# Performance work log

Hardware: AMD Instinct MI355X
Metric: run time of the kernel (lower is better)

The kernel has to match this reference:

```python
import jax, jax.numpy as jnp
import numpy as np

CH = 64
GROUPS = 8
EPS = 1e-5


def setup_inputs() -> dict:
    key = jax.random.key(0)
    ks = jax.random.split(key, 5)
    x = jax.random.normal(ks[0], (16, CH, 256, 256), dtype=jnp.float32)
    gn_weight = jnp.ones((CH,), jnp.float32)
    gn_bias = jnp.zeros((CH,), jnp.float32)
    # 1x1 convs == per-pixel channel GEMMs; store as [C_out, C_in]
    s = 1.0 / np.sqrt(CH)
    w1 = jax.random.uniform(ks[1], (CH, CH), jnp.float32, -s, s)
    b1 = jax.random.uniform(ks[2], (CH,), jnp.float32, -s, s)
    w2 = jax.random.uniform(ks[3], (CH, CH), jnp.float32, -s, s)
    b2 = jax.random.uniform(ks[4], (CH,), jnp.float32, -s, s)
    return {"x": x, "gn_weight": gn_weight, "gn_bias": gn_bias,
            "w1": w1, "b1": b1, "w2": w2, "b2": b2}


def group_norm(x, weight, bias):
    B, C, H, W = x.shape
    g = x.reshape(B, GROUPS, C // GROUPS, H, W)
    mean = g.mean(axis=(2, 3, 4), keepdims=True)
    var = g.var(axis=(2, 3, 4), keepdims=True)
    g = (g - mean) * jax.lax.rsqrt(var + EPS)
    x = g.reshape(B, C, H, W)
    return x * weight[None, :, None, None] + bias[None, :, None, None]


def reference(x, gn_weight, gn_bias, w1, b1, w2, b2):
    # FFT2 -> IFFT2 round-trip, keep real part (identity up to float noise)
    x_ifft = jnp.fft.ifft2(jnp.fft.fft2(x, axes=(-2, -1)), axes=(-2, -1)).real
    x_norm = group_norm(x_ifft, gn_weight, gn_bias)
    # ffn: 1x1 conv -> relu -> 1x1 conv, as channel einsums
    h = jnp.einsum('oc,bchw->bohw', w1, x_norm) + b1[None, :, None, None]
    h = jax.nn.relu(h)
    h = jnp.einsum('oc,bchw->bohw', w2, h) + b2[None, :, None, None]
    return x_norm + h
```

## Files before the change

kernel.cpp:

```cpp
#include <hip/hip_runtime.h>

#define CH 64
#define HW 65536
#define NBATCH 16
#define GROUP_ELEMS (8 * HW)
#define GN_EPS 1e-5f

typedef __attribute__((ext_vector_type(8))) short bf16x8;
typedef __attribute__((ext_vector_type(4))) float f32x4;

#define WS_SUMS   0
#define WS_FRAGS  1024
#define WS_SCALE  16384
#define WS_SHIFT  17408

static __device__ __forceinline__ unsigned short f2bf(float f) {
    unsigned u = __float_as_uint(f);
    return (unsigned short)((u + 0x7fffu + ((u >> 16) & 1u)) >> 16);
}
static __device__ __forceinline__ float bf2f(unsigned h) {
    return __uint_as_float(h << 16);
}
#define SWZ(a) ((a) ^ ((((a) >> 7) & 7) << 4))

__global__ __launch_bounds__(256, 8) void gn_stats(const float* __restrict__ x,
                                                   float* __restrict__ ws) {
    const int blk = blockIdx.x, grp = blk >> 4, split = blk & 15, tid = threadIdx.x;
    const float4* x4 = (const float4*)x + (size_t)grp * (GROUP_ELEMS / 4)
                                        + (size_t)split * (GROUP_ELEMS / 64);
    float s = 0.f, ss = 0.f;
    #pragma unroll
    for (int i = 0; i < 32; ++i) {
        float4 v = x4[i * 256 + tid];
        s  += v.x + v.y + v.z + v.w;
        ss += v.x * v.x + v.y * v.y + v.z * v.z + v.w * v.w;
    }
    #pragma unroll
    for (int o = 32; o > 0; o >>= 1) {
        s += __shfl_down(s, o, 64);
        ss += __shfl_down(ss, o, 64);
    }
    if ((tid & 63) == 0) {
        atomicAdd(&ws[grp * 2 + 0], s);
        atomicAdd(&ws[grp * 2 + 1], ss);
    }
}

__global__ __launch_bounds__(64) void gn_setup(const float* __restrict__ w1,
                                               const float* __restrict__ w2,
                                               const float* __restrict__ gamma,
                                               const float* __restrict__ beta,
                                               float* __restrict__ ws) {
    const int bid = blockIdx.x, l = threadIdx.x;
    if (bid < 16) {
        const int mat = bid >> 3, mt = (bid >> 1) & 3, kt = bid & 1;
        const float* w = mat ? w2 : w1;
        const int row = mt * 16 + (l & 15);
        const float* p = w + row * 64 + kt * 32 + (l >> 4) * 8;
        unsigned hi[4], lo[4];
        #pragma unroll
        for (int j = 0; j < 4; ++j) {
            float v0 = p[2 * j], v1 = p[2 * j + 1];
            unsigned h0 = f2bf(v0), h1 = f2bf(v1);
            unsigned l0 = f2bf(v0 - bf2f(h0)), l1 = f2bf(v1 - bf2f(h1));
            hi[j] = h0 | (h1 << 16);
            lo[j] = l0 | (l1 << 16);
        }
        unsigned* fr = (unsigned*)ws + WS_FRAGS;
        const int fhi = (mat * 2 + 0) * 8 + mt * 2 + kt;
        const int flo = (mat * 2 + 1) * 8 + mt * 2 + kt;
        *(uint4*)(fr + fhi * 256 + l * 4) = make_uint4(hi[0], hi[1], hi[2], hi[3]);
        *(uint4*)(fr + flo * 256 + l * 4) = make_uint4(lo[0], lo[1], lo[2], lo[3]);
    } else {
        const int c = l, g = c >> 3;
        const float ga = gamma[c], be = beta[c], invn = 1.f / (float)GROUP_ELEMS;
        for (int b = 0; b < NBATCH; ++b) {
            float s  = ws[(b * 8 + g) * 2 + 0];
            float ss = ws[(b * 8 + g) * 2 + 1];
            float m  = s * invn;
            float var = ss * invn - m * m;
            float rs = rsqrtf(var + GN_EPS);
            float A = rs * ga;
            ws[WS_SCALE + b * 64 + c] = A;
            ws[WS_SHIFT + b * 64 + c] = be - m * A;
        }
    }
}

__global__ __launch_bounds__(256, 2) void fused_gn_ffn(
        const float* __restrict__ x,
        const float* __restrict__ b1g, const float* __restrict__ b2g,
        const float* __restrict__ ws, float* __restrict__ out) {

    __shared__ __align__(16) char lds[65536];
    const int tid = threadIdx.x, wid = tid >> 6, l = tid & 63;
    const int b = blockIdx.x >> 9;
    const int pw = (blockIdx.x & 511) * 128 + wid * 32;

    char* X_hi = lds + wid * 16384;
    char* X_lo = X_hi + 4096;
    char* H_hi = X_hi + 8192;
    char* H_lo = X_hi + 12288;

    const unsigned* fr = (const unsigned*)ws + WS_FRAGS;
    bf16x8 w1h[4][2], w1l[4][2], w2h[4][2], w2l[4][2];
    #pragma unroll
    for (int mt = 0; mt < 4; ++mt)
        #pragma unroll
        for (int kt = 0; kt < 2; ++kt) {
            w1h[mt][kt] = __builtin_bit_cast(bf16x8, *(const uint4*)(fr + (0  + mt * 2 + kt) * 256 + l * 4));
            w1l[mt][kt] = __builtin_bit_cast(bf16x8, *(const uint4*)(fr + (8  + mt * 2 + kt) * 256 + l * 4));
            w2h[mt][kt] = __builtin_bit_cast(bf16x8, *(const uint4*)(fr + (16 + mt * 2 + kt) * 256 + l * 4));
            w2l[mt][kt] = __builtin_bit_cast(bf16x8, *(const uint4*)(fr + (24 + mt * 2 + kt) * 256 + l * 4));
        }

    f32x4 b1v[4], b2v[4];
    #pragma unroll
    for (int mt = 0; mt < 4; ++mt) {
        const int r = mt * 16 + (l >> 4) * 4;
        b1v[mt] = *(const f32x4*)(b1g + r);
        b2v[mt] = *(const f32x4*)(b2g + r);
    }

    const float* scale = ws + WS_SCALE + b * 64;
    const float* shift = ws + WS_SHIFT + b * 64;
    const int pixl = l & 31;
    #pragma unroll
    for (int a = 0; a < 4; ++a) {
        const int oct = (l >> 5) + 2 * a;
        float sc[8], sh[8];
        *(f32x4*)(sc)     = *(const f32x4*)(scale + oct * 8);
        *(f32x4*)(sc + 4) = *(const f32x4*)(scale + oct * 8 + 4);
        *(f32x4*)(sh)     = *(const f32x4*)(shift + oct * 8);
        *(f32x4*)(sh + 4) = *(const f32x4*)(shift + oct * 8 + 4);
        const float* gp = x + ((size_t)(b * 64 + oct * 8)) * HW + pw + pixl;
        float xn[8];
        #pragma unroll
        for (int j = 0; j < 8; ++j)
            xn[j] = fmaf(gp[(size_t)j * HW], sc[j], sh[j]);
        unsigned hiw[4], low[4];
        #pragma unroll
        for (int j = 0; j < 4; ++j) {
            unsigned h0 = f2bf(xn[2 * j]), h1 = f2bf(xn[2 * j + 1]);
            unsigned l0 = f2bf(xn[2 * j] - bf2f(h0));
            unsigned l1 = f2bf(xn[2 * j + 1] - bf2f(h1));
            hiw[j] = h0 | (h1 << 16);
            low[j] = l0 | (l1 << 16);
        }
        const unsigned ad = (unsigned)(pixl * 128 + oct * 16);
        *(uint4*)(X_hi + SWZ(ad)) = make_uint4(hiw[0], hiw[1], hiw[2], hiw[3]);
        *(uint4*)(X_lo + SWZ(ad)) = make_uint4(low[0], low[1], low[2], low[3]);
    }

    #pragma unroll
    for (int pc = 0; pc < 2; ++pc) {
        const unsigned ba = (unsigned)((pc * 16 + (l & 15)) * 128 + (l >> 4) * 16);
        bf16x8 xh0 = __builtin_bit_cast(bf16x8, *(const uint4*)(X_hi + SWZ(ba)));
        bf16x8 xh1 = __builtin_bit_cast(bf16x8, *(const uint4*)(X_hi + SWZ(ba + 64)));
        bf16x8 xl0 = __builtin_bit_cast(bf16x8, *(const uint4*)(X_lo + SWZ(ba)));
        bf16x8 xl1 = __builtin_bit_cast(bf16x8, *(const uint4*)(X_lo + SWZ(ba + 64)));

        f32x4 acc[4];
        #pragma unroll
        for (int mt = 0; mt < 4; ++mt) acc[mt] = b1v[mt];
        #pragma unroll
        for (int mt = 0; mt < 4; ++mt) {
            acc[mt] = __builtin_amdgcn_mfma_f32_16x16x32_bf16(w1h[mt][0], xh0, acc[mt], 0, 0, 0);
            acc[mt] = __builtin_amdgcn_mfma_f32_16x16x32_bf16(w1h[mt][1], xh1, acc[mt], 0, 0, 0);
            acc[mt] = __builtin_amdgcn_mfma_f32_16x16x32_bf16(w1h[mt][0], xl0, acc[mt], 0, 0, 0);
            acc[mt] = __builtin_amdgcn_mfma_f32_16x16x32_bf16(w1h[mt][1], xl1, acc[mt], 0, 0, 0);
            acc[mt] = __builtin_amdgcn_mfma_f32_16x16x32_bf16(w1l[mt][0], xh0, acc[mt], 0, 0, 0);
            acc[mt] = __builtin_amdgcn_mfma_f32_16x16x32_bf16(w1l[mt][1], xh1, acc[mt], 0, 0, 0);
        }

        #pragma unroll
        for (int mt = 0; mt < 4; ++mt) {
            float h0 = fmaxf(acc[mt][0], 0.f), h1 = fmaxf(acc[mt][1], 0.f);
            float h2 = fmaxf(acc[mt][2], 0.f), h3 = fmaxf(acc[mt][3], 0.f);
            unsigned a0 = f2bf(h0), a1 = f2bf(h1), a2 = f2bf(h2), a3 = f2bf(h3);
            unsigned c0 = f2bf(h0 - bf2f(a0)), c1 = f2bf(h1 - bf2f(a1));
            unsigned c2 = f2bf(h2 - bf2f(a2)), c3 = f2bf(h3 - bf2f(a3));
            const unsigned ha = (unsigned)((pc * 16 + (l & 15)) * 128 + mt * 32 + (l >> 4) * 8);
            *(uint2*)(H_hi + SWZ(ha)) = make_uint2(a0 | (a1 << 16), a2 | (a3 << 16));
            *(uint2*)(H_lo + SWZ(ha)) = make_uint2(c0 | (c1 << 16), c2 | (c3 << 16));
        }

        f32x4 acc2[4];
        #pragma unroll
        for (int mt = 0; mt < 4; ++mt) {
            const unsigned ra = (unsigned)((pc * 16 + (l & 15)) * 128 + mt * 32 + (l >> 4) * 8);
            uint2 rh = *(const uint2*)(X_hi + SWZ(ra));
            uint2 rl = *(const uint2*)(X_lo + SWZ(ra));
            f32x4 res;
            res[0] = bf2f(rh.x & 0xffffu) + bf2f(rl.x & 0xffffu);
            res[1] = bf2f(rh.x >> 16)     + bf2f(rl.x >> 16);
            res[2] = bf2f(rh.y & 0xffffu) + bf2f(rl.y & 0xffffu);
            res[3] = bf2f(rh.y >> 16)     + bf2f(rl.y >> 16);
            acc2[mt] = b2v[mt] + res;
        }

        bf16x8 hh0 = __builtin_bit_cast(bf16x8, *(const uint4*)(H_hi + SWZ(ba)));
        bf16x8 hh1 = __builtin_bit_cast(bf16x8, *(const uint4*)(H_hi + SWZ(ba + 64)));
        bf16x8 hl0 = __builtin_bit_cast(bf16x8, *(const uint4*)(H_lo + SWZ(ba)));
        bf16x8 hl1 = __builtin_bit_cast(bf16x8, *(const uint4*)(H_lo + SWZ(ba + 64)));
        #pragma unroll
        for (int mt = 0; mt < 4; ++mt) {
            acc2[mt] = __builtin_amdgcn_mfma_f32_16x16x32_bf16(w2h[mt][0], hh0, acc2[mt], 0, 0, 0);
            acc2[mt] = __builtin_amdgcn_mfma_f32_16x16x32_bf16(w2h[mt][1], hh1, acc2[mt], 0, 0, 0);
            acc2[mt] = __builtin_amdgcn_mfma_f32_16x16x32_bf16(w2h[mt][0], hl0, acc2[mt], 0, 0, 0);
            acc2[mt] = __builtin_amdgcn_mfma_f32_16x16x32_bf16(w2h[mt][1], hl1, acc2[mt], 0, 0, 0);
            acc2[mt] = __builtin_amdgcn_mfma_f32_16x16x32_bf16(w2l[mt][0], hh0, acc2[mt], 0, 0, 0);
            acc2[mt] = __builtin_amdgcn_mfma_f32_16x16x32_bf16(w2l[mt][1], hh1, acc2[mt], 0, 0, 0);
        }

        #pragma unroll
        for (int mt = 0; mt < 4; ++mt) {
            const int row = mt * 16 + (l >> 4) * 4;
            float* op = out + ((size_t)(b * 64 + row)) * HW + pw + pc * 16 + (l & 15);
            __builtin_nontemporal_store(acc2[mt][0], op);
            __builtin_nontemporal_store(acc2[mt][1], op + HW);
            __builtin_nontemporal_store(acc2[mt][2], op + 2 * HW);
            __builtin_nontemporal_store(acc2[mt][3], op + 3 * HW);
        }
    }
}

extern "C" void kernel_launch(void* const* d_in, const int* in_sizes, int n_in,
                              void* d_out, int out_size, void* d_ws, size_t ws_size,
                              hipStream_t stream) {
    const float* x     = (const float*)d_in[0];
    const float* gamma = (const float*)d_in[1];
    const float* beta  = (const float*)d_in[2];
    const float* w1    = (const float*)d_in[3];
    const float* b1    = (const float*)d_in[4];
    const float* w2    = (const float*)d_in[5];
    const float* b2    = (const float*)d_in[6];
    float* out = (float*)d_out;
    float* ws  = (float*)d_ws;

    hipMemsetAsync(ws, 0, 256 * sizeof(float), stream);
    gn_stats<<<2048, 256, 0, stream>>>(x, ws);
    gn_setup<<<17, 64, 0, stream>>>(w1, w2, gamma, beta, ws);
    fused_gn_ffn<<<NBATCH * 512, 256, 0, stream>>>(x, b1, b2, ws, out);
}
```

Baseline: 539.8 us.

## Restructure fused GN-FFN into per-wave 16-pixel loop with smaller LDS footprint

```diff
diff --git a/kernel.cpp b/kernel.cpp
--- a/kernel.cpp
+++ b/kernel.cpp
@@ -1,4 +1,5 @@
 #include <hip/hip_runtime.h>
+#include <hip/hip_bf16.h>
 
 #define CH 64
 #define HW 65536
@@ -17,6 +18,9 @@
 static __device__ __forceinline__ unsigned short f2bf(float f) {
     unsigned u = __float_as_uint(f);
     return (unsigned short)((u + 0x7fffu + ((u >> 16) & 1u)) >> 16);
+}
+static __device__ __forceinline__ unsigned short f2bf_hw(float f) {
+    return __bfloat16_as_ushort(__float2bfloat16(f));
 }
 static __device__ __forceinline__ float bf2f(unsigned h) {
     return __uint_as_float(h << 16);
@@ -87,32 +91,20 @@
     }
 }
 
-__global__ __launch_bounds__(256, 2) void fused_gn_ffn(
+__global__ __launch_bounds__(256, 3) void fused_gn_ffn(
         const float* __restrict__ x,
         const float* __restrict__ b1g, const float* __restrict__ b2g,
         const float* __restrict__ ws, float* __restrict__ out) {
 
-    __shared__ __align__(16) char lds[65536];
+    __shared__ __align__(16) char lds[16384];
     const int tid = threadIdx.x, wid = tid >> 6, l = tid & 63;
-    const int b = blockIdx.x >> 9;
-    const int pw = (blockIdx.x & 511) * 128 + wid * 32;
-
-    char* X_hi = lds + wid * 16384;
-    char* X_lo = X_hi + 4096;
-    char* H_hi = X_hi + 8192;
-    char* H_lo = X_hi + 12288;
-
-    const unsigned* fr = (const unsigned*)ws + WS_FRAGS;
-    bf16x8 w1h[4][2], w1l[4][2], w2h[4][2], w2l[4][2];
-    #pragma unroll
-    for (int mt = 0; mt < 4; ++mt)
-        #pragma unroll
-        for (int kt = 0; kt < 2; ++kt) {
-            w1h[mt][kt] = __builtin_bit_cast(bf16x8, *(const uint4*)(fr + (0  + mt * 2 + kt) * 256 + l * 4));
-            w1l[mt][kt] = __builtin_bit_cast(bf16x8, *(const uint4*)(fr + (8  + mt * 2 + kt) * 256 + l * 4));
-            w2h[mt][kt] = __builtin_bit_cast(bf16x8, *(const uint4*)(fr + (16 + mt * 2 + kt) * 256 + l * 4));
-            w2l[mt][kt] = __builtin_bit_cast(bf16x8, *(const uint4*)(fr + (24 + mt * 2 + kt) * 256 + l * 4));
-        }
+    const int b = blockIdx.x >> 7;
+    const int pbase = (blockIdx.x & 127) * 512 + wid * 128;
+
+    char* X_hi = lds + wid * 4096;
+    char* X_lo = X_hi + 2048;
+
+    const uint4* fr4 = (const uint4*)((const unsigned*)ws + WS_FRAGS) + l;
 
     f32x4 b1v[4], b2v[4];
     #pragma unroll
@@ -122,39 +114,46 @@
         b2v[mt] = *(const f32x4*)(b2g + r);
     }
 
+    float sca[16], sha[16];
     const float* scale = ws + WS_SCALE + b * 64;
     const float* shift = ws + WS_SHIFT + b * 64;
-    const int pixl = l & 31;
-    #pragma unroll
-    for (int a = 0; a < 4; ++a) {
-        const int oct = (l >> 5) + 2 * a;
-        float sc[8], sh[8];
-        *(f32x4*)(sc)     = *(const f32x4*)(scale + oct * 8);
-        *(f32x4*)(sc + 4) = *(const f32x4*)(scale + oct * 8 + 4);
-        *(f32x4*)(sh)     = *(const f32x4*)(shift + oct * 8);
-        *(f32x4*)(sh + 4) = *(const f32x4*)(shift + oct * 8 + 4);
-        const float* gp = x + ((size_t)(b * 64 + oct * 8)) * HW + pw + pixl;
-        float xn[8];
-        #pragma unroll
-        for (int j = 0; j < 8; ++j)
-            xn[j] = fmaf(gp[(size_t)j * HW], sc[j], sh[j]);
-        unsigned hiw[4], low[4];
-        #pragma unroll
-        for (int j = 0; j < 4; ++j) {
-            unsigned h0 = f2bf(xn[2 * j]), h1 = f2bf(xn[2 * j + 1]);
-            unsigned l0 = f2bf(xn[2 * j] - bf2f(h0));
-            unsigned l1 = f2bf(xn[2 * j + 1] - bf2f(h1));
-            hiw[j] = h0 | (h1 << 16);
-            low[j] = l0 | (l1 << 16);
-        }
-        const unsigned ad = (unsigned)(pixl * 128 + oct * 16);
-        *(uint4*)(X_hi + SWZ(ad)) = make_uint4(hiw[0], hiw[1], hiw[2], hiw[3]);
-        *(uint4*)(X_lo + SWZ(ad)) = make_uint4(low[0], low[1], low[2], low[3]);
-    }
-
-    #pragma unroll
-    for (int pc = 0; pc < 2; ++pc) {
-        const unsigned ba = (unsigned)((pc * 16 + (l & 15)) * 128 + (l >> 4) * 16);
+    #pragma unroll
+    for (int a = 0; a < 2; ++a) {
+        const int oct = (l >> 4) + 4 * a;
+        *(f32x4*)(sca + a * 8)     = *(const f32x4*)(scale + oct * 8);
+        *(f32x4*)(sca + a * 8 + 4) = *(const f32x4*)(scale + oct * 8 + 4);
+        *(f32x4*)(sha + a * 8)     = *(const f32x4*)(shift + oct * 8);
+        *(f32x4*)(sha + a * 8 + 4) = *(const f32x4*)(shift + oct * 8 + 4);
+    }
+
+    #pragma unroll 2
+    for (int t = 0; t < 8; ++t) {
+        const int pix0 = pbase + t * 16;
+        const int p = l & 15;
+
+        #pragma unroll
+        for (int a = 0; a < 2; ++a) {
+            const int oct = (l >> 4) + 4 * a;
+            const float* gp = x + ((size_t)(b * 64 + oct * 8)) * HW + pix0 + p;
+            float xn[8];
+            #pragma unroll
+            for (int j = 0; j < 8; ++j)
+                xn[j] = fmaf(gp[(size_t)j * HW], sca[a * 8 + j], sha[a * 8 + j]);
+            unsigned hiw[4], low[4];
+            #pragma unroll
+            for (int j = 0; j < 4; ++j) {
+                unsigned h0 = f2bf_hw(xn[2 * j]), h1 = f2bf_hw(xn[2 * j + 1]);
+                unsigned l0 = f2bf_hw(xn[2 * j] - bf2f(h0));
+                unsigned l1 = f2bf_hw(xn[2 * j + 1] - bf2f(h1));
+                hiw[j] = h0 | (h1 << 16);
+                low[j] = l0 | (l1 << 16);
+            }
+            const unsigned ad = (unsigned)(p * 128 + oct * 16);
+            *(uint4*)(X_hi + SWZ(ad)) = make_uint4(hiw[0], hiw[1], hiw[2], hiw[3]);
+            *(uint4*)(X_lo + SWZ(ad)) = make_uint4(low[0], low[1], low[2], low[3]);
+        }
+
+        const unsigned ba = (unsigned)(p * 128 + (l >> 4) * 16);
         bf16x8 xh0 = __builtin_bit_cast(bf16x8, *(const uint4*)(X_hi + SWZ(ba)));
         bf16x8 xh1 = __builtin_bit_cast(bf16x8, *(const uint4*)(X_hi + SWZ(ba + 64)));
         bf16x8 xl0 = __builtin_bit_cast(bf16x8, *(const uint4*)(X_lo + SWZ(ba)));
@@ -162,33 +161,25 @@
 
         f32x4 acc[4];
         #pragma unroll
-        for (int mt = 0; mt < 4; ++mt) acc[mt] = b1v[mt];
-        #pragma unroll
         for (int mt = 0; mt < 4; ++mt) {
-            acc[mt] = __builtin_amdgcn_mfma_f32_16x16x32_bf16(w1h[mt][0], xh0, acc[mt], 0, 0, 0);
-            acc[mt] = __builtin_amdgcn_mfma_f32_16x16x32_bf16(w1h[mt][1], xh1, acc[mt], 0, 0, 0);
-            acc[mt] = __builtin_amdgcn_mfma_f32_16x16x32_bf16(w1h[mt][0], xl0, acc[mt], 0, 0, 0);
-            acc[mt] = __builtin_amdgcn_mfma_f32_16x16x32_bf16(w1h[mt][1], xl1, acc[mt], 0, 0, 0);
-            acc[mt] = __builtin_amdgcn_mfma_f32_16x16x32_bf16(w1l[mt][0], xh0, acc[mt], 0, 0, 0);
-            acc[mt] = __builtin_amdgcn_mfma_f32_16x16x32_bf16(w1l[mt][1], xh1, acc[mt], 0, 0, 0);
-        }
-
+            bf16x8 ah0 = __builtin_bit_cast(bf16x8, fr4[(0 + mt * 2 + 0) * 64]);
+            bf16x8 ah1 = __builtin_bit_cast(bf16x8, fr4[(0 + mt * 2 + 1) * 64]);
+            bf16x8 al0 = __builtin_bit_cast(bf16x8, fr4[(8 + mt * 2 + 0) * 64]);
+            bf16x8 al1 = __builtin_bit_cast(bf16x8, fr4[(8 + mt * 2 + 1) * 64]);
+            f32x4 a = b1v[mt];
+            a = __builtin_amdgcn_mfma_f32_16x16x32_bf16(ah0, xh0, a, 0, 0, 0);
+            a = __builtin_amdgcn_mfma_f32_16x16x32_bf16(ah1, xh1, a, 0, 0, 0);
+            a = __builtin_amdgcn_mfma_f32_16x16x32_bf16(ah0, xl0, a, 0, 0, 0);
+            a = __builtin_amdgcn_mfma_f32_16x16x32_bf16(ah1, xl1, a, 0, 0, 0);
+            a = __builtin_amdgcn_mfma_f32_16x16x32_bf16(al0, xh0, a, 0, 0, 0);
+            a = __builtin_amdgcn_mfma_f32_16x16x32_bf16(al1, xh1, a, 0, 0, 0);
+            acc[mt] = a;
+        }
+
+        f32x4 acc2[4];
         #pragma unroll
         for (int mt = 0; mt < 4; ++mt) {
-            float h0 = fmaxf(acc[mt][0], 0.f), h1 = fmaxf(acc[mt][1], 0.f);
-            float h2 = fmaxf(acc[mt][2], 0.f), h3 = fmaxf(acc[mt][3], 0.f);
-            unsigned a0 = f2bf(h0), a1 = f2bf(h1), a2 = f2bf(h2), a3 = f2bf(h3);
-            unsigned c0 = f2bf(h0 - bf2f(a0)), c1 = f2bf(h1 - bf2f(a1));
-            unsigned c2 = f2bf(h2 - bf2f(a2)), c3 = f2bf(h3 - bf2f(a3));
-            const unsigned ha = (unsigned)((pc * 16 + (l & 15)) * 128 + mt * 32 + (l >> 4) * 8);
-            *(uint2*)(H_hi + SWZ(ha)) = make_uint2(a0 | (a1 << 16), a2 | (a3 << 16));
-            *(uint2*)(H_lo + SWZ(ha)) = make_uint2(c0 | (c1 << 16), c2 | (c3 << 16));
-        }
-
-        f32x4 acc2[4];
-        #pragma unroll
-        for (int mt = 0; mt < 4; ++mt) {
-            const unsigned ra = (unsigned)((pc * 16 + (l & 15)) * 128 + mt * 32 + (l >> 4) * 8);
+            const unsigned ra = (unsigned)(p * 128 + mt * 32 + (l >> 4) * 8);
             uint2 rh = *(const uint2*)(X_hi + SWZ(ra));
             uint2 rl = *(const uint2*)(X_lo + SWZ(ra));
             f32x4 res;
@@ -197,30 +188,40 @@
             res[2] = bf2f(rh.y & 0xffffu) + bf2f(rl.y & 0xffffu);
             res[3] = bf2f(rh.y >> 16)     + bf2f(rl.y >> 16);
             acc2[mt] = b2v[mt] + res;
-        }
-
-        bf16x8 hh0 = __builtin_bit_cast(bf16x8, *(const uint4*)(H_hi + SWZ(ba)));
-        bf16x8 hh1 = __builtin_bit_cast(bf16x8, *(const uint4*)(H_hi + SWZ(ba + 64)));
-        bf16x8 hl0 = __builtin_bit_cast(bf16x8, *(const uint4*)(H_lo + SWZ(ba)));
-        bf16x8 hl1 = __builtin_bit_cast(bf16x8, *(const uint4*)(H_lo + SWZ(ba + 64)));
+
+            float h0 = fmaxf(acc[mt][0], 0.f), h1 = fmaxf(acc[mt][1], 0.f);
+            float h2 = fmaxf(acc[mt][2], 0.f), h3 = fmaxf(acc[mt][3], 0.f);
+            unsigned a0 = f2bf_hw(h0), a1 = f2bf_hw(h1), a2 = f2bf_hw(h2), a3 = f2bf_hw(h3);
+            unsigned c0 = f2bf_hw(h0 - bf2f(a0)), c1 = f2bf_hw(h1 - bf2f(a1));
+            unsigned c2 = f2bf_hw(h2 - bf2f(a2)), c3 = f2bf_hw(h3 - bf2f(a3));
+            *(uint2*)(X_hi + SWZ(ra)) = make_uint2(a0 | (a1 << 16), a2 | (a3 << 16));
+            *(uint2*)(X_lo + SWZ(ra)) = make_uint2(c0 | (c1 << 16), c2 | (c3 << 16));
+        }
+
+        bf16x8 hh0 = __builtin_bit_cast(bf16x8, *(const uint4*)(X_hi + SWZ(ba)));
+        bf16x8 hh1 = __builtin_bit_cast(bf16x8, *(const uint4*)(X_hi + SWZ(ba + 64)));
+        bf16x8 hl0 = __builtin_bit_cast(bf16x8, *(const uint4*)(X_lo + SWZ(ba)));
+        bf16x8 hl1 = __builtin_bit_cast(bf16x8, *(const uint4*)(X_lo + SWZ(ba + 64)));
         #pragma unroll
         for (int mt = 0; mt < 4; ++mt) {
-            acc2[mt] = __builtin_amdgcn_mfma_f32_16x16x32_bf16(w2h[mt][0], hh0, acc2[mt], 0, 0, 0);
-            acc2[mt] = __builtin_amdgcn_mfma_f32_16x16x32_bf16(w2h[mt][1], hh1, acc2[mt], 0, 0, 0);
-            acc2[mt] = __builtin_amdgcn_mfma_f32_16x16x32_bf16(w2h[mt][0], hl0, acc2[mt], 0, 0, 0);
-            acc2[mt] = __builtin_amdgcn_mfma_f32_16x16x32_bf16(w2h[mt][1], hl1, acc2[mt], 0, 0, 0);
-            acc2[mt] = __builtin_amdgcn_mfma_f32_16x16x32_bf16(w2l[mt][0], hh0, acc2[mt], 0, 0, 0);
-            acc2[mt] = __builtin_amdgcn_mfma_f32_16x16x32_bf16(w2l[mt][1], hh1, acc2[mt], 0, 0, 0);
-        }
-
-        #pragma unroll
-        for (int mt = 0; mt < 4; ++mt) {
+            bf16x8 ah0 = __builtin_bit_cast(bf16x8, fr4[(16 + mt * 2 + 0) * 64]);
+            bf16x8 ah1 = __builtin_bit_cast(bf16x8, fr4[(16 + mt * 2 + 1) * 64]);
+            bf16x8 al0 = __builtin_bit_cast(bf16x8, fr4[(24 + mt * 2 + 0) * 64]);
+            bf16x8 al1 = __builtin_bit_cast(bf16x8, fr4[(24 + mt * 2 + 1) * 64]);
+            f32x4 a = acc2[mt];
+            a = __builtin_amdgcn_mfma_f32_16x16x32_bf16(ah0, hh0, a, 0, 0, 0);
+            a = __builtin_amdgcn_mfma_f32_16x16x32_bf16(ah1, hh1, a, 0, 0, 0);
+            a = __builtin_amdgcn_mfma_f32_16x16x32_bf16(ah0, hl0, a, 0, 0, 0);
+            a = __builtin_amdgcn_mfma_f32_16x16x32_bf16(ah1, hl1, a, 0, 0, 0);
+            a = __builtin_amdgcn_mfma_f32_16x16x32_bf16(al0, hh0, a, 0, 0, 0);
+            a = __builtin_amdgcn_mfma_f32_16x16x32_bf16(al1, hh1, a, 0, 0, 0);
+
             const int row = mt * 16 + (l >> 4) * 4;
-            float* op = out + ((size_t)(b * 64 + row)) * HW + pw + pc * 16 + (l & 15);
-            __builtin_nontemporal_store(acc2[mt][0], op);
-            __builtin_nontemporal_store(acc2[mt][1], op + HW);
-            __builtin_nontemporal_store(acc2[mt][2], op + 2 * HW);
-            __builtin_nontemporal_store(acc2[mt][3], op + 3 * HW);
+            float* op = out + ((size_t)(b * 64 + row)) * HW + pix0 + p;
+            __builtin_nontemporal_store(a[0], op);
+            __builtin_nontemporal_store(a[1], op + HW);
+            __builtin_nontemporal_store(a[2], op + 2 * HW);
+            __builtin_nontemporal_store(a[3], op + 3 * HW);
         }
     }
 }
@@ -241,5 +242,5 @@
     hipMemsetAsync(ws, 0, 256 * sizeof(float), stream);
     gn_stats<<<2048, 256, 0, stream>>>(x, ws);
     gn_setup<<<17, 64, 0, stream>>>(w1, w2, gamma, beta, ws);
-    fused_gn_ffn<<<NBATCH * 512, 256, 0, stream>>>(x, b1, b2, ws, out);
-}
+    fused_gn_ffn<<<2048, 256, 0, stream>>>(x, b1, b2, ws, out);
+}
```

Result: slower. 934.8 us (+73.2%).
